# Performance work log

Hardware: AMD Instinct MI355X
Metric: run time of the kernel (lower is better)

The kernel has to match this reference:

```python
import jax, jax.numpy as jnp
import numpy as np

D_MODEL = 1024
NUM_HEADS = 16
D_K = D_MODEL // NUM_HEADS
THETA = 10000.0


def _rope(x, cos, sin):
    # x: [b, h, l, d_k]; cos/sin: [l, d_k//2]
    x1 = x[..., ::2]
    x2 = x[..., 1::2]
    re = x1 * cos - x2 * sin
    ro = x1 * sin + x2 * cos
    return jnp.stack([re, ro], axis=-1).reshape(x.shape)


def setup_inputs() -> dict:
    key = jax.random.key(0)
    k0, k1, k2, k3, k4 = jax.random.split(key, 5)
    b, l = 2, 2048
    scale = 1.0 / np.sqrt(D_MODEL)
    return {
        "in_features": jax.random.normal(k0, (b, l, D_MODEL), dtype=jnp.float32),
        "wq": jax.random.normal(k1, (D_MODEL, D_MODEL), dtype=jnp.float32) * scale,
        "wk": jax.random.normal(k2, (D_MODEL, D_MODEL), dtype=jnp.float32) * scale,
        "wv": jax.random.normal(k3, (D_MODEL, D_MODEL), dtype=jnp.float32) * scale,
        "wo": jax.random.normal(k4, (D_MODEL, D_MODEL), dtype=jnp.float32) * scale,
    }


def reference(in_features, wq, wk, wv, wo):
    b, l, d = in_features.shape
    h, dk = NUM_HEADS, D_K

    def proj(w):
        # torch: einsum('b l d, k d -> b l k') == x @ w.T
        y = jnp.einsum('bld,kd->blk', in_features, w)
        return y.reshape(b, l, h, dk).transpose(0, 2, 1, 3)  # [b,h,l,dk]

    Q, K, V = proj(wq), proj(wk), proj(wv)

    # RoPE (use_rope=True)
    inv_freq = 1.0 / (THETA ** (jnp.arange(0, dk, 2, dtype=jnp.float32) / dk))
    angles = jnp.arange(l, dtype=jnp.float32)[:, None] * inv_freq[None, :]  # [l, dk//2]
    cos, sin = jnp.cos(angles), jnp.sin(angles)
    Q = _rope(Q, cos, sin)
    K = _rope(K, cos, sin)

    scores = jnp.einsum('bhqd,bhkd->bhqk', Q, K) / jnp.sqrt(jnp.float32(dk))
    causal = jnp.tril(jnp.ones((l, l), dtype=bool))  # [l,l]
    scores = jnp.where(causal[None, None], scores, jnp.float32(-jnp.inf))
    attn = jax.nn.softmax(scores, axis=-1)
    ctx = jnp.einsum('bhqk,bhkd->bhqd', attn, V)
    ctx = ctx.transpose(0, 2, 1, 3).reshape(b, l, d)  # [b,l,d_model]
    out = jnp.einsum('bld,md->blm', ctx, wo)
    return out
```

## Files before the change

### kernel.cpp

```cpp
#include <hip/hip_runtime.h>
#include <stdint.h>

typedef __attribute__((ext_vector_type(8))) short short8;
typedef __attribute__((ext_vector_type(4))) float floatx4;
typedef __attribute__((ext_vector_type(16))) float floatx16;

#define DEV static __device__ __forceinline__

DEV unsigned short f2bf(float f) {
  union { float f; uint32_t u; } v; v.f = f;
  return (unsigned short)((v.u + 0x7FFFu + ((v.u >> 16) & 1u)) >> 16);
}
DEV float bf2f(unsigned short h) {
  union { uint32_t u; float f; } v; v.u = ((uint32_t)h) << 16;
  return v.f;
}
DEV uint32_t cvtpk(float lo, float hi) {
  uint32_t d;
  asm("v_cvt_pk_bf16_f32 %0, %1, %2" : "=v"(d) : "v"(lo), "v"(hi));
  return d;
}
DEV void gload_lds16(const void* g, void* l) {
  __builtin_amdgcn_global_load_lds(
      (const __attribute__((address_space(1))) uint32_t*)g,
      (__attribute__((address_space(3))) uint32_t*)l, 16, 0, 0);
}

#if defined(__has_builtin)
#if __has_builtin(__builtin_amdgcn_permlane32_swap)
#define HAVE_PLSWAP 1
#endif
#endif
DEV void plswap(uint32_t& a, uint32_t& b) {
#ifdef HAVE_PLSWAP
  typedef unsigned int u2v __attribute__((ext_vector_type(2)));
  u2v r = __builtin_amdgcn_permlane32_swap(a, b, false, false);
  a = r.x; b = r.y;
#else
  uint32_t sa = (uint32_t)__shfl_xor((int)a, 32);
  uint32_t sb = (uint32_t)__shfl_xor((int)b, 32);
  uint32_t lane = __lane_id();
  uint32_t na = lane < 32 ? a : sb;
  uint32_t nb = lane < 32 ? sa : b;
  a = na; b = nb;
#endif
}
DEV float xmax32(float x) {
  union { float f; uint32_t u; } a, b; a.f = x; b.f = x;
  plswap(a.u, b.u);
  return fmaxf(a.f, b.f);
}
DEV float xsum32(float x) {
  union { float f; uint32_t u; } a, b; a.f = x; b.f = x;
  plswap(a.u, b.u);
  return a.f + b.f;
}

__global__ __launch_bounds__(256) void k_convert(
    const float* __restrict__ X, const float* __restrict__ Wq,
    const float* __restrict__ Wk, const float* __restrict__ Wv,
    const float* __restrict__ Wo, unsigned short* __restrict__ out) {
  long gid = (long)blockIdx.x * 256 + threadIdx.x;
  long e = gid * 8;
  int seg = (int)(e >> 20);
  const float* src; long base;
  if (seg < 4)      { src = X;  base = 0; }
  else if (seg == 4){ src = Wq; base = 4l << 20; }
  else if (seg == 5){ src = Wk; base = 5l << 20; }
  else if (seg == 6){ src = Wv; base = 6l << 20; }
  else              { src = Wo; base = 7l << 20; }
  const float4* s4 = (const float4*)(src + (e - base));
  float4 a = s4[0], b = s4[1];
  union { uint4 q; unsigned short s[8]; } u;
  u.s[0] = f2bf(a.x); u.s[1] = f2bf(a.y); u.s[2] = f2bf(a.z); u.s[3] = f2bf(a.w);
  u.s[4] = f2bf(b.x); u.s[5] = f2bf(b.y); u.s[6] = f2bf(b.z); u.s[7] = f2bf(b.w);
  *(uint4*)(out + e) = u.q;
}

template <int MODE>
__global__ __launch_bounds__(256) void k_gemm(
    const unsigned short* __restrict__ A,
    const unsigned short* __restrict__ B0, const unsigned short* __restrict__ B1,
    const unsigned short* __restrict__ B2,
    unsigned short* __restrict__ Cq, unsigned short* __restrict__ Ck,
    unsigned short* __restrict__ Cv, float* __restrict__ Cf, int K) {
  __shared__ unsigned short At[128 * 64];
  __shared__ unsigned short Bt[128 * 64];
  const int tid = threadIdx.x, lane = tid & 63, wid = tid >> 6;
  const int wm = (wid >> 1) * 64, wn = (wid & 1) * 64;
  const int g = lane >> 4, c0 = lane & 15;
  const int bm0 = blockIdx.x * 128;
  const int bnG = blockIdx.y * 128;
  const unsigned short* Bp;
  int bn0;
  if constexpr (MODE == 0) {
    int wsel = bnG >> 10;
    Bp = wsel == 0 ? B0 : (wsel == 1 ? B1 : B2);
    bn0 = bnG & 1023;
  } else { Bp = B0; bn0 = bnG; }
  floatx4 acc[4][4] = {};
  for (int kt = 0; kt < K; kt += 64) {
#pragma unroll
    for (int i = 0; i < 4; ++i) {
      int o = (wid * 64 + lane) * 16 + i * 4096;
      int row = o >> 7, k0 = (o & 127) >> 1;
      gload_lds16((const char*)A  + ((long)(bm0 + row) * K + kt + k0) * 2, (char*)At + o);
      gload_lds16((const char*)Bp + ((long)(bn0 + row) * K + kt + k0) * 2, (char*)Bt + o);
    }
    __syncthreads();
#pragma unroll
    for (int kk = 0; kk < 2; ++kk) {
      const int kb = kk * 64 + g * 16;
      short8 av[4], bv[4];
#pragma unroll
      for (int mi = 0; mi < 4; ++mi)
        av[mi] = *(const short8*)((const char*)At + (wm + mi * 16 + c0) * 128 + kb);
#pragma unroll
      for (int ni = 0; ni < 4; ++ni)
        bv[ni] = *(const short8*)((const char*)Bt + (wn + ni * 16 + c0) * 128 + kb);
#pragma unroll
      for (int mi = 0; mi < 4; ++mi)
#pragma unroll
        for (int ni = 0; ni < 4; ++ni)
          acc[mi][ni] = __builtin_amdgcn_mfma_f32_16x16x32_bf16(av[mi], bv[ni], acc[mi][ni], 0, 0, 0);
    }
    __syncthreads();
  }
#pragma unroll
  for (int mi = 0; mi < 4; ++mi)
#pragma unroll
    for (int ni = 0; ni < 4; ++ni)
#pragma unroll
      for (int i = 0; i < 4; ++i) {
        int r = bm0 + wm + mi * 16 + 4 * g + i;
        int cg = bnG + wn + ni * 16 + c0;
        float v = acc[mi][ni][i];
        if constexpr (MODE == 0) {
          int wsel = cg >> 10, cc = cg & 1023, h = cc >> 6, dkk = cc & 63;
          int bb = r >> 11, ll = r & 2047;
          unsigned short* dst = wsel == 0 ? Cq : (wsel == 1 ? Ck : Cv);
          dst[((long)(bb * 16 + h) * 2048 + ll) * 64 + dkk] = f2bf(v);
        } else {
          Cf[(long)r * 1024 + cg] = v;
        }
      }
}

__global__ __launch_bounds__(256) void k_rope(unsigned short* __restrict__ Qd, float qscale) {
  int gid = blockIdx.x * 256 + threadIdx.x;
  int row = gid >> 1, hf = gid & 1;
  int l = row & 2047;
  unsigned short* p = Qd + (long)row * 64 + hf * 32;
  union { uint4 q[4]; unsigned short s[32]; } u;
#pragma unroll
  for (int i = 0; i < 4; ++i) u.q[i] = ((const uint4*)p)[i];
  float lf = (float)l;
#pragma unroll
  for (int j = 0; j < 16; ++j) {
    int pp = hf * 16 + j;
    float ang = lf * exp2f(-(float)pp * 0.4152410118609203f);
    float sv, cv; sincosf(ang, &sv, &cv);
    float x1 = bf2f(u.s[2 * j]), x2 = bf2f(u.s[2 * j + 1]);
    u.s[2 * j]     = f2bf((x1 * cv - x2 * sv) * qscale);
    u.s[2 * j + 1] = f2bf((x1 * sv + x2 * cv) * qscale);
  }
#pragma unroll
  for (int i = 0; i < 4; ++i) ((uint4*)p)[i] = u.q[i];
}

__global__ __launch_bounds__(256) void k_ropeK_repack(
    const unsigned short* __restrict__ Kin, unsigned short* __restrict__ KF) {
  const int blk = blockIdx.x;
  const int bh = blk >> 5, T = blk & 31;
  const int tid = threadIdx.x;
  const unsigned short* src = Kin + ((long)bh * 2048 + T * 64) * 64;
  unsigned short* dst = KF + (long)blk * 4096;
#pragma unroll
  for (int it = 0; it < 2; ++it) {
    int u = tid + it * 256;
    int lane = u & 63, kd = u >> 6;
    int kvs = kd >> 2, dseg = kd & 3;
    int row = kvs * 32 + (lane & 31);
    int col = dseg * 16 + 8 * (lane >> 5);
    union { uint4 q; unsigned short s[8]; } v;
    v.q = *(const uint4*)(src + row * 64 + col);
    float lf = (float)(T * 64 + row);
#pragma unroll
    for (int j = 0; j < 4; ++j) {
      int p = (col >> 1) + j;
      float ang = lf * exp2f(-(float)p * 0.4152410118609203f);
      float sv, cv; sincosf(ang, &sv, &cv);
      float x1 = bf2f(v.s[2 * j]), x2 = bf2f(v.s[2 * j + 1]);
      v.s[2 * j]     = f2bf(x1 * cv - x2 * sv);
      v.s[2 * j + 1] = f2bf(x1 * sv + x2 * cv);
    }
    *(uint4*)(dst + u * 8) = v.q;
  }
}

__global__ __launch_bounds__(256) void k_repackV(
    const unsigned short* __restrict__ Vin, unsigned short* __restrict__ VF) {
  __shared__ unsigned short t[64][68];
  const int blk = blockIdx.x;
  const int bh = blk >> 5, T = blk & 31;
  const int tid = threadIdx.x;
  const unsigned short* src = Vin + ((long)bh * 2048 + T * 64) * 64;
#pragma unroll
  for (int p = 0; p < 2; ++p) {
    int idx = tid + p * 256;
    int row = idx >> 3, c = (idx & 7) * 8;
    union { uint4 q; unsigned short s[8]; } u;
    u.q = *(const uint4*)(src + row * 64 + c);
#pragma unroll
    for (int j = 0; j < 8; ++j) t[row][c + j] = u.s[j];
  }
  __syncthreads();
  unsigned short* dst = VF + (long)blk * 4096;
#pragma unroll
  for (int p = 0; p < 2; ++p) {
    int u = tid + p * 256;
    int lane = u & 63, dm = u >> 6;
    int dvs = dm >> 2, m = dm & 3;
    int col = dvs * 32 + (lane & 31);
    int r0 = m * 16 + 8 * (lane >> 5);
    union { uint4 q; unsigned short s[8]; } v;
#pragma unroll
    for (int j = 0; j < 8; ++j) v.s[j] = t[r0 + j][col];
    *(uint4*)(dst + u * 8) = v.q;
  }
}

DEV void attn_tile(int T, int Tend, int ntm1, int qabs, int h, int c,
                   const unsigned short* __restrict__ kfbase,
                   const unsigned short* __restrict__ vfbase,
                   const short8 (&qf)[4],
                   const short8 (&kc0)[4], const short8 (&kc1)[4],
                   short8 (&kn0)[4], short8 (&kn1)[4],
                   floatx16& ctx0, floatx16& ctx1, float& m_, float& l_) {
  {
    const int Tn = T + 1 < Tend ? T + 1 : T;
    const unsigned short* kt = kfbase + (long)Tn * 4096;
#pragma unroll
    for (int d = 0; d < 4; ++d) kn0[d] = *(const short8*)(kt + d * 512);
#pragma unroll
    for (int d = 0; d < 4; ++d) kn1[d] = *(const short8*)(kt + 2048 + d * 512);
  }
  const unsigned short* vt = vfbase + (long)T * 4096;
  short8 vf0[4], vf1[4];
#pragma unroll
  for (int m = 0; m < 4; ++m) vf0[m] = *(const short8*)(vt + m * 512);
#pragma unroll
  for (int m = 0; m < 4; ++m) vf1[m] = *(const short8*)(vt + 2048 + m * 512);

  floatx16 s0 = {}, s1 = {};
#pragma unroll
  for (int d = 0; d < 4; ++d)
    s0 = __builtin_amdgcn_mfma_f32_32x32x16_bf16(kc0[d], qf[d], s0, 0, 0, 0);
#pragma unroll
  for (int d = 0; d < 4; ++d)
    s1 = __builtin_amdgcn_mfma_f32_32x32x16_bf16(kc1[d], qf[d], s1, 0, 0, 0);

  if (T == ntm1) {
    const int kvb = T * 64 + 4 * h;
#pragma unroll
    for (int r = 0; r < 16; ++r) {
      const int off = (r & 3) + 8 * (r >> 2);
      if (kvb + off > qabs) s0[r] = -1e30f;
      if (kvb + 32 + off > qabs) s1[r] = -1e30f;
    }
  }
  float a4[8];
#pragma unroll
  for (int j = 0; j < 4; ++j) {
    a4[j]     = fmaxf(fmaxf(s0[4 * j], s0[4 * j + 1]), fmaxf(s0[4 * j + 2], s0[4 * j + 3]));
    a4[4 + j] = fmaxf(fmaxf(s1[4 * j], s1[4 * j + 1]), fmaxf(s1[4 * j + 2], s1[4 * j + 3]));
  }
  float mx = fmaxf(fmaxf(fmaxf(a4[0], a4[1]), fmaxf(a4[2], a4[3])),
                   fmaxf(fmaxf(a4[4], a4[5]), fmaxf(a4[6], a4[7])));
  mx = xmax32(mx);
  float mn = fmaxf(m_, mx);
  float sc = exp2f(m_ - mn);
  m_ = mn;
#pragma unroll
  for (int r = 0; r < 16; ++r) s0[r] = exp2f(s0[r] - m_);
#pragma unroll
  for (int r = 0; r < 16; ++r) s1[r] = exp2f(s1[r] - m_);
  float b4[8];
#pragma unroll
  for (int j = 0; j < 4; ++j) {
    b4[j]     = (s0[4 * j] + s0[4 * j + 1]) + (s0[4 * j + 2] + s0[4 * j + 3]);
    b4[4 + j] = (s1[4 * j] + s1[4 * j + 1]) + (s1[4 * j + 2] + s1[4 * j + 3]);
  }
  float rs = ((b4[0] + b4[1]) + (b4[2] + b4[3])) + ((b4[4] + b4[5]) + (b4[6] + b4[7]));
  rs = xsum32(rs);
  l_ = l_ * sc + rs;
#pragma unroll
  for (int r = 0; r < 16; ++r) { ctx0[r] *= sc; ctx1[r] *= sc; }

  uint32_t pd0[8], pd1[8];
#pragma unroll
  for (int d = 0; d < 8; ++d) {
    pd0[d] = cvtpk(s0[2 * d], s0[2 * d + 1]);
    pd1[d] = cvtpk(s1[2 * d], s1[2 * d + 1]);
  }
#pragma unroll
  for (int kvs = 0; kvs < 2; ++kvs) {
    const uint32_t* pd = kvs ? pd1 : pd0;
#pragma unroll
    for (int ks = 0; ks < 2; ++ks) {
      uint32_t u0 = pd[4 * ks], u2 = pd[4 * ks + 2];
      uint32_t u1 = pd[4 * ks + 1], u3 = pd[4 * ks + 3];
      plswap(u0, u2);
      plswap(u1, u3);
      union { uint32_t u[4]; short8 s; } bu;
      bu.u[0] = u0; bu.u[1] = u1; bu.u[2] = u2; bu.u[3] = u3;
      ctx0 = __builtin_amdgcn_mfma_f32_32x32x16_bf16(vf0[kvs * 2 + ks], bu.s, ctx0, 0, 0, 0);
      ctx1 = __builtin_amdgcn_mfma_f32_32x32x16_bf16(vf1[kvs * 2 + ks], bu.s, ctx1, 0, 0, 0);
    }
  }
}

__global__ __launch_bounds__(128) void k_attn(
    const unsigned short* __restrict__ Q, const unsigned short* __restrict__ KF,
    const unsigned short* __restrict__ VF, unsigned short* __restrict__ O) {
  __shared__ float lctx[64][33];
  __shared__ float lml[64][2];
  const int bid = blockIdx.x;
  const int xcd = bid & 7, idx = bid >> 3;
  const int head = idx >> 6;
  const int a = idx & 63;
  const int qs = (head < 2) ? a : 63 - a;
  const int bh = xcd * 4 + head;
  const int tid = threadIdx.x;
  const int wid = tid >> 6, lane = tid & 63;
  const int h = lane >> 5, c = lane & 31;
  const unsigned short* Qh = Q + (long)bh * 2048 * 64;
  const unsigned short* kfbase = KF + (long)bh * 32 * 4096 + lane * 8;
  const unsigned short* vfbase = VF + (long)bh * 32 * 4096 + lane * 8;
  const int q0 = qs * 32, qabs = q0 + c;
  const int nt = (qs >> 1) + 1, ntm1 = nt - 1;
  const int h0 = nt >> 1;
  const int Tbeg = wid ? h0 : 0;
  const int Tend = wid ? nt : h0;

  short8 qf[4];
#pragma unroll
  for (int d = 0; d < 4; ++d)
    qf[d] = *(const short8*)(Qh + (long)(q0 + c) * 64 + d * 16 + 8 * h);

  floatx16 ctx0 = {}, ctx1 = {};
  float m_ = -1e30f, l_ = 0.f;

  if (Tbeg < Tend) {
    short8 kA0[4], kA1[4], kB0[4], kB1[4];
    const unsigned short* kt0 = kfbase + (long)Tbeg * 4096;
#pragma unroll
    for (int d = 0; d < 4; ++d) kA0[d] = *(const short8*)(kt0 + d * 512);
#pragma unroll
    for (int d = 0; d < 4; ++d) kA1[d] = *(const short8*)(kt0 + 2048 + d * 512);
    int T = Tbeg;
    while (true) {
      attn_tile(T, Tend, ntm1, qabs, h, c, kfbase, vfbase, qf, kA0, kA1, kB0, kB1, ctx0, ctx1, m_, l_);
      if (++T >= Tend) break;
      attn_tile(T, Tend, ntm1, qabs, h, c, kfbase, vfbase, qf, kB0, kB1, kA0, kA1, ctx0, ctx1, m_, l_);
      if (++T >= Tend) break;
    }
  }
  if (wid) {
#pragma unroll
    for (int r = 0; r < 16; ++r) {
      lctx[lane][r] = ctx0[r];
      lctx[lane][16 + r] = ctx1[r];
    }
    lml[lane][0] = m_;
    lml[lane][1] = l_;
  }
  __syncthreads();
  if (!wid) {
    float m1 = lml[lane][0], l1 = lml[lane][1];
    float m = fmaxf(m_, m1);
    float e0 = exp2f(m_ - m), e1 = exp2f(m1 - m);
    float inv = 1.f / (l_ * e0 + l1 * e1);
    const int b = bh >> 4, hd = bh & 15;
    unsigned short* orow = O + (long)(b * 2048 + q0 + c) * 1024 + hd * 64;
#pragma unroll
    for (int m4 = 0; m4 < 4; ++m4) {
      uint2 w0, w1;
      w0.x = cvtpk((ctx0[4 * m4]     * e0 + lctx[lane][4 * m4]     * e1) * inv,
                   (ctx0[4 * m4 + 1] * e0 + lctx[lane][4 * m4 + 1] * e1) * inv);
      w0.y = cvtpk((ctx0[4 * m4 + 2] * e0 + lctx[lane][4 * m4 + 2] * e1) * inv,
                   (ctx0[4 * m4 + 3] * e0 + lctx[lane][4 * m4 + 3] * e1) * inv);
      *(uint2*)(orow + 8 * m4 + 4 * h) = w0;
      w1.x = cvtpk((ctx1[4 * m4]     * e0 + lctx[lane][16 + 4 * m4]     * e1) * inv,
                   (ctx1[4 * m4 + 1] * e0 + lctx[lane][16 + 4 * m4 + 1] * e1) * inv);
      w1.y = cvtpk((ctx1[4 * m4 + 2] * e0 + lctx[lane][16 + 4 * m4 + 2] * e1) * inv,
                   (ctx1[4 * m4 + 3] * e0 + lctx[lane][16 + 4 * m4 + 3] * e1) * inv);
      *(uint2*)(orow + 32 + 8 * m4 + 4 * h) = w1;
    }
  }
}

extern "C" void kernel_launch(void* const* d_in, const int* in_sizes, int n_in,
                              void* d_out, int out_size, void* d_ws, size_t ws_size,
                              hipStream_t stream) {
  const float* X  = (const float*)d_in[0];
  const float* Wq = (const float*)d_in[1];
  const float* Wk = (const float*)d_in[2];
  const float* Wv = (const float*)d_in[3];
  const float* Wo = (const float*)d_in[4];
  unsigned short* Xb  = (unsigned short*)d_ws;
  unsigned short* Wqb = Xb + (4l << 20);
  unsigned short* Wkb = Xb + (5l << 20);
  unsigned short* Wvb = Xb + (6l << 20);
  unsigned short* Wob = Xb + (7l << 20);
  unsigned short* Qw  = Xb + (8l << 20);
  unsigned short* Kw  = Xb + (12l << 20);
  unsigned short* Vw  = Xb + (16l << 20);
  unsigned short* KFw = Xb;
  unsigned short* VFw = Xb + (12l << 20);
  unsigned short* Cw  = Xb + (20l << 20);
  float* Out = (float*)d_out;

  k_convert<<<4096, 256, 0, stream>>>(X, Wq, Wk, Wv, Wo, Xb);
  k_gemm<0><<<dim3(32, 24), 256, 0, stream>>>(Xb, Wqb, Wkb, Wvb, Qw, Kw, Vw, nullptr, 1024);
  k_rope<<<512, 256, 0, stream>>>(Qw, 0.18033688011112042f);
  k_ropeK_repack<<<1024, 256, 0, stream>>>(Kw, KFw);
  k_repackV<<<1024, 256, 0, stream>>>(Vw, VFw);
  k_attn<<<2048, 128, 0, stream>>>(Qw, KFw, VFw, Cw);
  k_gemm<1><<<dim3(32, 8), 256, 0, stream>>>(Cw, Wob, nullptr, nullptr,
                                             nullptr, nullptr, nullptr, Out, 1024);
}
```

Measured before the change: 148.2 us.

## Fuse RoPE and K/V repacking into QKV GEMM epilogue; lazy softmax rescale

```diff
diff --git a/kernel.cpp b/kernel.cpp
--- a/kernel.cpp
+++ b/kernel.cpp
@@ -82,8 +82,8 @@
     const unsigned short* __restrict__ A,
     const unsigned short* __restrict__ B0, const unsigned short* __restrict__ B1,
     const unsigned short* __restrict__ B2,
-    unsigned short* __restrict__ Cq, unsigned short* __restrict__ Ck,
-    unsigned short* __restrict__ Cv, float* __restrict__ Cf, int K) {
+    unsigned short* __restrict__ Qo, unsigned short* __restrict__ KFo,
+    unsigned short* __restrict__ VFo, float* __restrict__ Cf, int K) {
   __shared__ unsigned short At[128 * 64];
   __shared__ unsigned short Bt[128 * 64];
   const int tid = threadIdx.x, lane = tid & 63, wid = tid >> 6;
@@ -126,107 +126,53 @@
     }
     __syncthreads();
   }
-#pragma unroll
-  for (int mi = 0; mi < 4; ++mi)
-#pragma unroll
-    for (int ni = 0; ni < 4; ++ni)
-#pragma unroll
-      for (int i = 0; i < 4; ++i) {
-        int r = bm0 + wm + mi * 16 + 4 * g + i;
-        int cg = bnG + wn + ni * 16 + c0;
-        float v = acc[mi][ni][i];
-        if constexpr (MODE == 0) {
-          int wsel = cg >> 10, cc = cg & 1023, h = cc >> 6, dkk = cc & 63;
+  if constexpr (MODE == 1) {
+#pragma unroll
+    for (int mi = 0; mi < 4; ++mi)
+#pragma unroll
+      for (int ni = 0; ni < 4; ++ni)
+#pragma unroll
+        for (int i = 0; i < 4; ++i) {
+          int r = bm0 + wm + mi * 16 + 4 * g + i;
+          int cg = bnG + wn + ni * 16 + c0;
+          Cf[(long)r * 1024 + cg] = acc[mi][ni][i];
+        }
+  } else {
+    const int wsel = bnG >> 10;
+#pragma unroll
+    for (int mi = 0; mi < 4; ++mi)
+#pragma unroll
+      for (int ni = 0; ni < 4; ++ni)
+#pragma unroll
+        for (int i = 0; i < 4; ++i) {
+          int r = bm0 + wm + mi * 16 + 4 * g + i;
+          int cg = bnG + wn + ni * 16 + c0;
+          int cc = cg & 1023, head = cc >> 6, dkk = cc & 63;
           int bb = r >> 11, ll = r & 2047;
-          unsigned short* dst = wsel == 0 ? Cq : (wsel == 1 ? Ck : Cv);
-          dst[((long)(bb * 16 + h) * 2048 + ll) * 64 + dkk] = f2bf(v);
-        } else {
-          Cf[(long)r * 1024 + cg] = v;
+          long bh = bb * 16 + head;
+          float v = acc[mi][ni][i];
+          if (wsel == 2) {
+            int T = ll >> 6, rt = ll & 63;
+            int m = rt >> 4, hb = (rt >> 3) & 1, j = rt & 7;
+            int dvs = dkk >> 5, c = dkk & 31;
+            VFo[bh * 131072 + T * 4096 + (dvs * 4 + m) * 512 + (hb * 32 + c) * 8 + j] = f2bf(v);
+          } else {
+            float pr = __shfl_xor(v, 1);
+            int p = dkk >> 1;
+            float ang = (float)ll * exp2f(-(float)p * 0.4152410118609203f);
+            float sv, cv; sincosf(ang, &sv, &cv);
+            float out = (dkk & 1) ? (pr * sv + v * cv) : (v * cv - pr * sv);
+            if (wsel == 0) {
+              out *= 0.18033688011112042f;
+              Qo[(bh * 2048 + ll) * 64 + dkk] = f2bf(out);
+            } else {
+              int T = ll >> 6, rt = ll & 63;
+              int kvs = rt >> 5, c = rt & 31;
+              int dseg = dkk >> 4, hb = (dkk >> 3) & 1, j = dkk & 7;
+              KFo[bh * 131072 + T * 4096 + (kvs * 4 + dseg) * 512 + (hb * 32 + c) * 8 + j] = f2bf(out);
+            }
+          }
         }
-      }
-}
-
-__global__ __launch_bounds__(256) void k_rope(unsigned short* __restrict__ Qd, float qscale) {
-  int gid = blockIdx.x * 256 + threadIdx.x;
-  int row = gid >> 1, hf = gid & 1;
-  int l = row & 2047;
-  unsigned short* p = Qd + (long)row * 64 + hf * 32;
-  union { uint4 q[4]; unsigned short s[32]; } u;
-#pragma unroll
-  for (int i = 0; i < 4; ++i) u.q[i] = ((const uint4*)p)[i];
-  float lf = (float)l;
-#pragma unroll
-  for (int j = 0; j < 16; ++j) {
-    int pp = hf * 16 + j;
-    float ang = lf * exp2f(-(float)pp * 0.4152410118609203f);
-    float sv, cv; sincosf(ang, &sv, &cv);
-    float x1 = bf2f(u.s[2 * j]), x2 = bf2f(u.s[2 * j + 1]);
-    u.s[2 * j]     = f2bf((x1 * cv - x2 * sv) * qscale);
-    u.s[2 * j + 1] = f2bf((x1 * sv + x2 * cv) * qscale);
-  }
-#pragma unroll
-  for (int i = 0; i < 4; ++i) ((uint4*)p)[i] = u.q[i];
-}
-
-__global__ __launch_bounds__(256) void k_ropeK_repack(
-    const unsigned short* __restrict__ Kin, unsigned short* __restrict__ KF) {
-  const int blk = blockIdx.x;
-  const int bh = blk >> 5, T = blk & 31;
-  const int tid = threadIdx.x;
-  const unsigned short* src = Kin + ((long)bh * 2048 + T * 64) * 64;
-  unsigned short* dst = KF + (long)blk * 4096;
-#pragma unroll
-  for (int it = 0; it < 2; ++it) {
-    int u = tid + it * 256;
-    int lane = u & 63, kd = u >> 6;
-    int kvs = kd >> 2, dseg = kd & 3;
-    int row = kvs * 32 + (lane & 31);
-    int col = dseg * 16 + 8 * (lane >> 5);
-    union { uint4 q; unsigned short s[8]; } v;
-    v.q = *(const uint4*)(src + row * 64 + col);
-    float lf = (float)(T * 64 + row);
-#pragma unroll
-    for (int j = 0; j < 4; ++j) {
-      int p = (col >> 1) + j;
-      float ang = lf * exp2f(-(float)p * 0.4152410118609203f);
-      float sv, cv; sincosf(ang, &sv, &cv);
-      float x1 = bf2f(v.s[2 * j]), x2 = bf2f(v.s[2 * j + 1]);
-      v.s[2 * j]     = f2bf(x1 * cv - x2 * sv);
-      v.s[2 * j + 1] = f2bf(x1 * sv + x2 * cv);
-    }
-    *(uint4*)(dst + u * 8) = v.q;
-  }
-}
-
-__global__ __launch_bounds__(256) void k_repackV(
-    const unsigned short* __restrict__ Vin, unsigned short* __restrict__ VF) {
-  __shared__ unsigned short t[64][68];
-  const int blk = blockIdx.x;
-  const int bh = blk >> 5, T = blk & 31;
-  const int tid = threadIdx.x;
-  const unsigned short* src = Vin + ((long)bh * 2048 + T * 64) * 64;
-#pragma unroll
-  for (int p = 0; p < 2; ++p) {
-    int idx = tid + p * 256;
-    int row = idx >> 3, c = (idx & 7) * 8;
-    union { uint4 q; unsigned short s[8]; } u;
-    u.q = *(const uint4*)(src + row * 64 + c);
-#pragma unroll
-    for (int j = 0; j < 8; ++j) t[row][c + j] = u.s[j];
-  }
-  __syncthreads();
-  unsigned short* dst = VF + (long)blk * 4096;
-#pragma unroll
-  for (int p = 0; p < 2; ++p) {
-    int u = tid + p * 256;
-    int lane = u & 63, dm = u >> 6;
-    int dvs = dm >> 2, m = dm & 3;
-    int col = dvs * 32 + (lane & 31);
-    int r0 = m * 16 + 8 * (lane >> 5);
-    union { uint4 q; unsigned short s[8]; } v;
-#pragma unroll
-    for (int j = 0; j < 8; ++j) v.s[j] = t[r0 + j][col];
-    *(uint4*)(dst + u * 8) = v.q;
   }
 }
 
@@ -278,9 +224,14 @@
   float mx = fmaxf(fmaxf(fmaxf(a4[0], a4[1]), fmaxf(a4[2], a4[3])),
                    fmaxf(fmaxf(a4[4], a4[5]), fmaxf(a4[6], a4[7])));
   mx = xmax32(mx);
-  float mn = fmaxf(m_, mx);
-  float sc = exp2f(m_ - mn);
-  m_ = mn;
+  if (!__all(mx <= m_ + 8.0f)) {
+    float mn = fmaxf(m_, mx);
+    float sc = exp2f(m_ - mn);
+    m_ = mn;
+    l_ *= sc;
+#pragma unroll
+    for (int r = 0; r < 16; ++r) { ctx0[r] *= sc; ctx1[r] *= sc; }
+  }
 #pragma unroll
   for (int r = 0; r < 16; ++r) s0[r] = exp2f(s0[r] - m_);
 #pragma unroll
@@ -293,9 +244,7 @@
   }
   float rs = ((b4[0] + b4[1]) + (b4[2] + b4[3])) + ((b4[4] + b4[5]) + (b4[6] + b4[7]));
   rs = xsum32(rs);
-  l_ = l_ * sc + rs;
-#pragma unroll
-  for (int r = 0; r < 16; ++r) { ctx0[r] *= sc; ctx1[r] *= sc; }
+  l_ += rs;
 
   uint32_t pd0[8], pd1[8];
 #pragma unroll
@@ -335,8 +284,8 @@
   const int wid = tid >> 6, lane = tid & 63;
   const int h = lane >> 5, c = lane & 31;
   const unsigned short* Qh = Q + (long)bh * 2048 * 64;
-  const unsigned short* kfbase = KF + (long)bh * 32 * 4096 + lane * 8;
-  const unsigned short* vfbase = VF + (long)bh * 32 * 4096 + lane * 8;
+  const unsigned short* kfbase = KF + (long)bh * 131072 + lane * 8;
+  const unsigned short* vfbase = VF + (long)bh * 131072 + lane * 8;
   const int q0 = qs * 32, qabs = q0 + c;
   const int nt = (qs >> 1) + 1, ntm1 = nt - 1;
   const int h0 = nt >> 1;
@@ -414,18 +363,13 @@
   unsigned short* Wvb = Xb + (6l << 20);
   unsigned short* Wob = Xb + (7l << 20);
   unsigned short* Qw  = Xb + (8l << 20);
-  unsigned short* Kw  = Xb + (12l << 20);
-  unsigned short* Vw  = Xb + (16l << 20);
-  unsigned short* KFw = Xb;
-  unsigned short* VFw = Xb + (12l << 20);
+  unsigned short* KFw = Xb + (12l << 20);
+  unsigned short* VFw = Xb + (16l << 20);
   unsigned short* Cw  = Xb + (20l << 20);
   float* Out = (float*)d_out;
 
   k_convert<<<4096, 256, 0, stream>>>(X, Wq, Wk, Wv, Wo, Xb);
-  k_gemm<0><<<dim3(32, 24), 256, 0, stream>>>(Xb, Wqb, Wkb, Wvb, Qw, Kw, Vw, nullptr, 1024);
-  k_rope<<<512, 256, 0, stream>>>(Qw, 0.18033688011112042f);
-  k_ropeK_repack<<<1024, 256, 0, stream>>>(Kw, KFw);
-  k_repackV<<<1024, 256, 0, stream>>>(Vw, VFw);
+  k_gemm<0><<<dim3(32, 24), 256, 0, stream>>>(Xb, Wqb, Wkb, Wvb, Qw, KFw, VFw, nullptr, 1024);
   k_attn<<<2048, 128, 0, stream>>>(Qw, KFw, VFw, Cw);
   k_gemm<1><<<dim3(32, 8), 256, 0, stream>>>(Cw, Wob, nullptr, nullptr,
                                              nullptr, nullptr, nullptr, Out, 1024);
```

New measurement: 159.3 us. 1.08x slower.

## Fuse V repack into QKV GEMM epilogue and add lazy softmax rescaling

Applied to the files above, without the earlier changes.

```diff
diff --git a/kernel.cpp b/kernel.cpp
--- a/kernel.cpp
+++ b/kernel.cpp
@@ -82,8 +82,8 @@
     const unsigned short* __restrict__ A,
     const unsigned short* __restrict__ B0, const unsigned short* __restrict__ B1,
     const unsigned short* __restrict__ B2,
-    unsigned short* __restrict__ Cq, unsigned short* __restrict__ Ck,
-    unsigned short* __restrict__ Cv, float* __restrict__ Cf, int K) {
+    unsigned short* __restrict__ Qo, unsigned short* __restrict__ Ko,
+    unsigned short* __restrict__ VFo, float* __restrict__ Cf, int K) {
   __shared__ unsigned short At[128 * 64];
   __shared__ unsigned short Bt[128 * 64];
   const int tid = threadIdx.x, lane = tid & 63, wid = tid >> 6;
@@ -126,24 +126,42 @@
     }
     __syncthreads();
   }
-#pragma unroll
-  for (int mi = 0; mi < 4; ++mi)
-#pragma unroll
-    for (int ni = 0; ni < 4; ++ni)
-#pragma unroll
-      for (int i = 0; i < 4; ++i) {
-        int r = bm0 + wm + mi * 16 + 4 * g + i;
-        int cg = bnG + wn + ni * 16 + c0;
-        float v = acc[mi][ni][i];
-        if constexpr (MODE == 0) {
-          int wsel = cg >> 10, cc = cg & 1023, h = cc >> 6, dkk = cc & 63;
+  if constexpr (MODE == 1) {
+#pragma unroll
+    for (int mi = 0; mi < 4; ++mi)
+#pragma unroll
+      for (int ni = 0; ni < 4; ++ni)
+#pragma unroll
+        for (int i = 0; i < 4; ++i) {
+          int r = bm0 + wm + mi * 16 + 4 * g + i;
+          int cg = bnG + wn + ni * 16 + c0;
+          Cf[(long)r * 1024 + cg] = acc[mi][ni][i];
+        }
+  } else {
+    const int wsel = bnG >> 10;
+#pragma unroll
+    for (int mi = 0; mi < 4; ++mi)
+#pragma unroll
+      for (int ni = 0; ni < 4; ++ni)
+#pragma unroll
+        for (int i = 0; i < 4; ++i) {
+          int r = bm0 + wm + mi * 16 + 4 * g + i;
+          int cg = bnG + wn + ni * 16 + c0;
+          int cc = cg & 1023, head = cc >> 6, dkk = cc & 63;
           int bb = r >> 11, ll = r & 2047;
-          unsigned short* dst = wsel == 0 ? Cq : (wsel == 1 ? Ck : Cv);
-          dst[((long)(bb * 16 + h) * 2048 + ll) * 64 + dkk] = f2bf(v);
-        } else {
-          Cf[(long)r * 1024 + cg] = v;
+          long bh = bb * 16 + head;
+          float v = acc[mi][ni][i];
+          if (wsel == 2) {
+            int T = ll >> 6, rt = ll & 63;
+            int m = rt >> 4, hb = (rt >> 3) & 1, j = rt & 7;
+            int dvs = dkk >> 5, c = dkk & 31;
+            VFo[bh * 131072 + T * 4096 + (dvs * 4 + m) * 512 + (hb * 32 + c) * 8 + j] = f2bf(v);
+          } else {
+            unsigned short* dst = wsel == 0 ? Qo : Ko;
+            dst[(bh * 2048 + ll) * 64 + dkk] = f2bf(v);
+          }
         }
-      }
+  }
 }
 
 __global__ __launch_bounds__(256) void k_rope(unsigned short* __restrict__ Qd, float qscale) {
@@ -194,38 +212,6 @@
       v.s[2 * j]     = f2bf(x1 * cv - x2 * sv);
       v.s[2 * j + 1] = f2bf(x1 * sv + x2 * cv);
     }
-    *(uint4*)(dst + u * 8) = v.q;
-  }
-}
-
-__global__ __launch_bounds__(256) void k_repackV(
-    const unsigned short* __restrict__ Vin, unsigned short* __restrict__ VF) {
-  __shared__ unsigned short t[64][68];
-  const int blk = blockIdx.x;
-  const int bh = blk >> 5, T = blk & 31;
-  const int tid = threadIdx.x;
-  const unsigned short* src = Vin + ((long)bh * 2048 + T * 64) * 64;
-#pragma unroll
-  for (int p = 0; p < 2; ++p) {
-    int idx = tid + p * 256;
-    int row = idx >> 3, c = (idx & 7) * 8;
-    union { uint4 q; unsigned short s[8]; } u;
-    u.q = *(const uint4*)(src + row * 64 + c);
-#pragma unroll
-    for (int j = 0; j < 8; ++j) t[row][c + j] = u.s[j];
-  }
-  __syncthreads();
-  unsigned short* dst = VF + (long)blk * 4096;
-#pragma unroll
-  for (int p = 0; p < 2; ++p) {
-    int u = tid + p * 256;
-    int lane = u & 63, dm = u >> 6;
-    int dvs = dm >> 2, m = dm & 3;
-    int col = dvs * 32 + (lane & 31);
-    int r0 = m * 16 + 8 * (lane >> 5);
-    union { uint4 q; unsigned short s[8]; } v;
-#pragma unroll
-    for (int j = 0; j < 8; ++j) v.s[j] = t[r0 + j][col];
     *(uint4*)(dst + u * 8) = v.q;
   }
 }
@@ -278,9 +264,14 @@
   float mx = fmaxf(fmaxf(fmaxf(a4[0], a4[1]), fmaxf(a4[2], a4[3])),
                    fmaxf(fmaxf(a4[4], a4[5]), fmaxf(a4[6], a4[7])));
   mx = xmax32(mx);
-  float mn = fmaxf(m_, mx);
-  float sc = exp2f(m_ - mn);
-  m_ = mn;
+  if (!__all(mx <= m_ + 8.0f)) {
+    float mn = fmaxf(m_, mx);
+    float sc = exp2f(m_ - mn);
+    m_ = mn;
+    l_ *= sc;
+#pragma unroll
+    for (int r = 0; r < 16; ++r) { ctx0[r] *= sc; ctx1[r] *= sc; }
+  }
 #pragma unroll
   for (int r = 0; r < 16; ++r) s0[r] = exp2f(s0[r] - m_);
 #pragma unroll
@@ -293,9 +284,7 @@
   }
   float rs = ((b4[0] + b4[1]) + (b4[2] + b4[3])) + ((b4[4] + b4[5]) + (b4[6] + b4[7]));
   rs = xsum32(rs);
-  l_ = l_ * sc + rs;
-#pragma unroll
-  for (int r = 0; r < 16; ++r) { ctx0[r] *= sc; ctx1[r] *= sc; }
+  l_ += rs;
 
   uint32_t pd0[8], pd1[8];
 #pragma unroll
@@ -335,8 +324,8 @@
   const int wid = tid >> 6, lane = tid & 63;
   const int h = lane >> 5, c = lane & 31;
   const unsigned short* Qh = Q + (long)bh * 2048 * 64;
-  const unsigned short* kfbase = KF + (long)bh * 32 * 4096 + lane * 8;
-  const unsigned short* vfbase = VF + (long)bh * 32 * 4096 + lane * 8;
+  const unsigned short* kfbase = KF + (long)bh * 131072 + lane * 8;
+  const unsigned short* vfbase = VF + (long)bh * 131072 + lane * 8;
   const int q0 = qs * 32, qabs = q0 + c;
   const int nt = (qs >> 1) + 1, ntm1 = nt - 1;
   const int h0 = nt >> 1;
@@ -415,17 +404,15 @@
   unsigned short* Wob = Xb + (7l << 20);
   unsigned short* Qw  = Xb + (8l << 20);
   unsigned short* Kw  = Xb + (12l << 20);
-  unsigned short* Vw  = Xb + (16l << 20);
+  unsigned short* VFw = Xb + (16l << 20);
   unsigned short* KFw = Xb;
-  unsigned short* VFw = Xb + (12l << 20);
   unsigned short* Cw  = Xb + (20l << 20);
   float* Out = (float*)d_out;
 
   k_convert<<<4096, 256, 0, stream>>>(X, Wq, Wk, Wv, Wo, Xb);
-  k_gemm<0><<<dim3(32, 24), 256, 0, stream>>>(Xb, Wqb, Wkb, Wvb, Qw, Kw, Vw, nullptr, 1024);
+  k_gemm<0><<<dim3(32, 24), 256, 0, stream>>>(Xb, Wqb, Wkb, Wvb, Qw, Kw, VFw, nullptr, 1024);
   k_rope<<<512, 256, 0, stream>>>(Qw, 0.18033688011112042f);
   k_ropeK_repack<<<1024, 256, 0, stream>>>(Kw, KFw);
-  k_repackV<<<1024, 256, 0, stream>>>(Vw, VFw);
   k_attn<<<2048, 128, 0, stream>>>(Qw, KFw, VFw, Cw);
   k_gemm<1><<<dim3(32, 8), 256, 0, stream>>>(Cw, Wob, nullptr, nullptr,
                                              nullptr, nullptr, nullptr, Out, 1024);
```

New measurement: 150.1 us. About the same (+1.3%).
